# Optimization experiments

Measured on AMD Instinct MI355X. Metric: run time of the kernel, lower is better.

The kernel has to match this reference:

```python
import jax, jax.numpy as jnp
import numpy as np

E, D, H, R = 8, 2048, 8192, 64   # experts, d_model(in=out), hidden, rank
N = 4096                          # tokens (batch*seq)


def setup_inputs() -> dict:
    key = jax.random.key(0)
    ks = jax.random.split(key, 8)
    f32 = jnp.float32
    x = jax.random.normal(ks[0], (N, D), f32)
    # Stacked low-rank expert params: expert i = relu(x@u1@v1+b1) @ u2 @ v2 + b2
    u1 = jax.random.normal(ks[1], (E, D, R), f32) / np.float32(np.sqrt(D))
    v1 = jax.random.normal(ks[2], (E, R, H), f32) / np.float32(np.sqrt(R))
    b1 = jnp.zeros((E, H), f32)
    u2 = jax.random.normal(ks[3], (E, H, R), f32) / np.float32(np.sqrt(H))
    v2 = jax.random.normal(ks[4], (E, R, D), f32) / np.float32(np.sqrt(R))
    b2 = jnp.zeros((E, D), f32)
    # gate = nn.Linear(D, E): weight [E, D], bias [E]
    gate_w = jax.random.normal(ks[5], (E, D), f32) / np.float32(np.sqrt(D))
    gate_b = jnp.zeros((E,), f32)
    return dict(x=x, u1=u1, v1=v1, b1=b1, u2=u2, v2=v2, b2=b2,
                gate_w=gate_w, gate_b=gate_b)


def reference(x, u1, v1, b1, u2, v2, b2, gate_w, gate_b):
    # --- routing: softmax gate, top-2, renormalize ---
    logits = x @ gate_w.T + gate_b                      # [N, E]
    probs = jax.nn.softmax(logits, axis=-1)
    top_p, top_i = jax.lax.top_k(probs, 2)              # [N, 2]
    top_p = top_p / jnp.sum(top_p, axis=-1, keepdims=True)
    # combine weight per (token, expert): zero unless expert in top-2
    w = jnp.sum(jax.nn.one_hot(top_i, E, dtype=x.dtype) * top_p[..., None], axis=1)  # [N, E]

    # --- experts: low-rank MLP applied per expert, weighted accumulate ---
    def body(acc, params):
        u1e, v1e, b1e, u2e, v2e, b2e, we = params       # we: [N]
        h = jax.nn.relu((x @ u1e) @ v1e + b1e)          # [N, H]
        y = (h @ u2e) @ v2e + b2e                       # [N, D]
        return acc + we[:, None] * y, None

    out, _ = jax.lax.scan(body, jnp.zeros_like(x), (u1, v1, b1, u2, v2, b2, w.T))
    return out
```

## Files before the change

kernel.cpp:

```cpp
#include <hip/hip_runtime.h>
#include <hip/hip_bf16.h>

#define E 8
#define D 2048
#define H 8192
#define R 64
#define NTOK 4096
#define HSPLIT 4
#define HPER (H / HSPLIT)

typedef __attribute__((ext_vector_type(8))) short bf16x8;
typedef __attribute__((ext_vector_type(4))) float f32x4;

__device__ __forceinline__ unsigned short f2b(float f){
  union { __hip_bfloat16 h; unsigned short u; } cv;
  cv.h = __float2bfloat16(f);
  return cv.u;
}
__device__ __forceinline__ float b2f(unsigned short u){
  union { unsigned int i; float f; } cv; cv.i = ((unsigned int)u) << 16; return cv.f;
}

__device__ __forceinline__ bf16x8 ldfrag(const unsigned short* base, int row0, int k0,
                                         int pitch, int lane){
  return *reinterpret_cast<const bf16x8*>(base + (row0 + (lane & 15)) * pitch
                                          + k0 + ((lane >> 4) << 3));
}

__global__ __launch_bounds__(256) void pack_tr(const float* __restrict__ src,
                                               unsigned short* __restrict__ dst,
                                               int RS, int CS){
  int e = blockIdx.z;
  const float* s = src + (size_t)e * RS * CS;
  unsigned short* d = dst + (size_t)e * RS * CS;
  int c0 = blockIdx.x * 64, r0 = blockIdx.y * 64;
  int l = threadIdx.x & 63, cb = (threadIdx.x >> 6) * 16;
  int r = r0 + l;
  const float4* sp = reinterpret_cast<const float4*>(s + (size_t)r * CS + c0 + cb);
  float v[16];
  #pragma unroll
  for (int q = 0; q < 4; ++q){
    float4 t = sp[q];
    v[q*4] = t.x; v[q*4+1] = t.y; v[q*4+2] = t.z; v[q*4+3] = t.w;
  }
  #pragma unroll
  for (int j = 0; j < 16; ++j)
    d[(size_t)(c0 + cb + j) * RS + r] = f2b(v[j]);
}

__global__ __launch_bounds__(256) void gate_kernel(
    const float* __restrict__ x, const float* __restrict__ gw,
    const float* __restrict__ gb, int* __restrict__ cnt,
    int* __restrict__ lst, int* __restrict__ tsl,
    unsigned short* __restrict__ xb)
{
  int wid  = threadIdx.x >> 6;
  int lane = threadIdx.x & 63;
  int n0 = blockIdx.x * 16 + wid * 4;

  float acc[4][E];
  #pragma unroll
  for (int t = 0; t < 4; ++t)
    #pragma unroll
    for (int e = 0; e < E; ++e) acc[t][e] = 0.f;

  for (int i = 0; i < D / 256; ++i){
    int dd = i * 256 + lane * 4;
    float4 xv[4];
    #pragma unroll
    for (int t = 0; t < 4; ++t){
      xv[t] = *reinterpret_cast<const float4*>(x + (size_t)(n0 + t) * D + dd);
      unsigned short o[4] = { f2b(xv[t].x), f2b(xv[t].y), f2b(xv[t].z), f2b(xv[t].w) };
      *reinterpret_cast<ushort4*>(xb + (size_t)(n0 + t) * D + dd) = *reinterpret_cast<ushort4*>(o);
    }
    #pragma unroll
    for (int e = 0; e < E; ++e){
      float4 g = *reinterpret_cast<const float4*>(gw + (size_t)e * D + dd);
      #pragma unroll
      for (int t = 0; t < 4; ++t)
        acc[t][e] += xv[t].x * g.x + xv[t].y * g.y + xv[t].z * g.z + xv[t].w * g.w;
    }
  }

  #pragma unroll
  for (int t = 0; t < 4; ++t){
    #pragma unroll
    for (int e = 0; e < E; ++e){
      float v = acc[t][e];
      for (int off = 32; off; off >>= 1) v += __shfl_xor(v, off, 64);
      acc[t][e] = v + gb[e];
    }
    if (lane == 0){
      int n = n0 + t;
      float l0 = -1e30f, l1 = -1e30f; int i0 = 0, i1 = 0;
      #pragma unroll
      for (int e = 0; e < E; ++e){
        float v = acc[t][e];
        if (v > l0){ l1 = l0; i1 = i0; l0 = v; i0 = e; }
        else if (v > l1){ l1 = v; i1 = e; }
      }
      float tt = expf(l1 - l0);
      float w0 = 1.f / (1.f + tt);
      float w1 = tt * w0;
      int p0 = atomicAdd(&cnt[i0], 1);
      lst[i0 * NTOK + p0] = n;
      int p1 = atomicAdd(&cnt[i1], 1);
      lst[i1 * NTOK + p1] = n;
      int* ts = tsl + n * 8;
      ts[0] = i0; ts[1] = p0; ts[2] = __float_as_int(w0);
      ts[3] = i1; ts[4] = p1; ts[5] = __float_as_int(w1);
    }
  }
}

__global__ __launch_bounds__(256) void t1_kernel(
    const unsigned short* __restrict__ xb, const unsigned short* __restrict__ u1p,
    const int* __restrict__ cnt, const int* __restrict__ lst,
    unsigned short* __restrict__ T1buf)
{
  int e = blockIdx.y;
  int nc = cnt[e];
  int t0 = blockIdx.x * 64;
  if (t0 >= nc) return;

  __shared__ int s_tok[64];
  __shared__ unsigned short Xs[64 * 136];
  __shared__ unsigned short U1s[64 * 136];
  int tid = threadIdx.x, w = tid >> 6, lane = tid & 63;

  if (tid < 64) s_tok[tid] = lst[e * NTOK + min(t0 + tid, nc - 1)];
  __syncthreads();

  int m = (w & 3) * 16;
  f32x4 z = {0.f, 0.f, 0.f, 0.f};
  f32x4 acc[4] = {z, z, z, z};

  for (int kc = 0; kc < D; kc += 128){
    __syncthreads();
    #pragma unroll
    for (int s = 0; s < 4; ++s){
      int id = tid + s * 256;
      int rr = id >> 4, c = (id & 15) * 8;
      *reinterpret_cast<bf16x8*>(&Xs[rr * 136 + c]) =
        *reinterpret_cast<const bf16x8*>(&xb[(size_t)s_tok[rr] * D + kc + c]);
      *reinterpret_cast<bf16x8*>(&U1s[rr * 136 + c]) =
        *reinterpret_cast<const bf16x8*>(&u1p[((size_t)e * R + rr) * D + kc + c]);
    }
    __syncthreads();
    #pragma unroll
    for (int j = 0; j < 4; ++j)
      #pragma unroll
      for (int ks = 0; ks < 4; ++ks)
        acc[j] = __builtin_amdgcn_mfma_f32_16x16x32_bf16(
            ldfrag(Xs, m, ks * 32, 136, lane),
            ldfrag(U1s, j * 16, ks * 32, 136, lane), acc[j], 0, 0, 0);
  }
  #pragma unroll
  for (int j = 0; j < 4; ++j){
    int col = j * 16 + (lane & 15);
    #pragma unroll
    for (int q = 0; q < 4; ++q){
      int row = m + ((lane >> 4) << 2) + q;
      T1buf[((size_t)e * NTOK + t0 + row) * R + col] = f2b(acc[j][q]);
    }
  }
}

__global__ __launch_bounds__(512, 4) void mid_kernel(
    const unsigned short* __restrict__ T1buf, const unsigned short* __restrict__ v1p,
    const unsigned short* __restrict__ u2p, const float* __restrict__ b1,
    const int* __restrict__ cnt, float* __restrict__ T2acc)
{
  int e = blockIdx.z;
  int nc = cnt[e];
  int t0 = blockIdx.x * 64;
  if (t0 >= nc) return;
  int hc0 = blockIdx.y * HPER;

  __shared__ unsigned short T1s[64 * 72];
  __shared__ unsigned short v1s[128 * 72];
  __shared__ unsigned short u2s[64 * 136];
  __shared__ unsigned short Hs[64 * 136];
  __shared__ float b1s[HPER];

  int tid = threadIdx.x, w = tid >> 6, lane = tid & 63;

  { int rr = tid >> 3, c = (tid & 7) * 8;
    *reinterpret_cast<bf16x8*>(&T1s[rr * 72 + c]) =
      *reinterpret_cast<const bf16x8*>(&T1buf[((size_t)e * NTOK + t0 + rr) * R + c]); }
  for (int i = tid; i < HPER; i += 512) b1s[i] = b1[(size_t)e * H + hc0 + i];

  int m1 = (w & 1) * 32, n1 = (w >> 1) * 32;
  int m2 = (w & 3) * 16, r2 = (w >> 2) * 32;
  f32x4 z = {0.f, 0.f, 0.f, 0.f};
  f32x4 acc[2] = {z, z};

  bf16x8 pv[2], pu[2];
  #pragma unroll
  for (int s = 0; s < 2; ++s){
    int id = tid + s * 512;
    pv[s] = *reinterpret_cast<const bf16x8*>(&v1p[((size_t)e * H + hc0 + (id >> 3)) * R + (id & 7) * 8]);
    pu[s] = *reinterpret_cast<const bf16x8*>(&u2p[((size_t)e * R + (id >> 4)) * H + hc0 + (id & 15) * 8]);
  }

  for (int hs = 0; hs < HPER; hs += 128){
    __syncthreads();
    #pragma unroll
    for (int s = 0; s < 2; ++s){
      int id = tid + s * 512;
      *reinterpret_cast<bf16x8*>(&v1s[(id >> 3) * 72 + (id & 7) * 8]) = pv[s];
      *reinterpret_cast<bf16x8*>(&u2s[(id >> 4) * 136 + (id & 15) * 8]) = pu[s];
    }
    __syncthreads();
    #pragma unroll
    for (int i = 0; i < 2; ++i)
      #pragma unroll
      for (int j = 0; j < 2; ++j){
        f32x4 a = z;
        #pragma unroll
        for (int ks = 0; ks < 2; ++ks)
          a = __builtin_amdgcn_mfma_f32_16x16x32_bf16(
              ldfrag(T1s, m1 + i * 16, ks * 32, 72, lane),
              ldfrag(v1s, n1 + j * 16, ks * 32, 72, lane), a, 0, 0, 0);
        int hcol = n1 + j * 16 + (lane & 15);
        float bv = b1s[hs + hcol];
        #pragma unroll
        for (int q = 0; q < 4; ++q){
          float vv = a[q] + bv;
          Hs[(m1 + i * 16 + ((lane >> 4) << 2) + q) * 136 + hcol] = f2b(vv > 0.f ? vv : 0.f);
        }
      }
    int hn = (hs + 128 < HPER) ? hs + 128 : 0;
    #pragma unroll
    for (int s = 0; s < 2; ++s){
      int id = tid + s * 512;
      pv[s] = *reinterpret_cast<const bf16x8*>(&v1p[((size_t)e * H + hc0 + hn + (id >> 3)) * R + (id & 7) * 8]);
      pu[s] = *reinterpret_cast<const bf16x8*>(&u2p[((size_t)e * R + (id >> 4)) * H + hc0 + hn + (id & 15) * 8]);
    }
    __syncthreads();
    #pragma unroll
    for (int j = 0; j < 2; ++j)
      #pragma unroll
      for (int ks = 0; ks < 4; ++ks)
        acc[j] = __builtin_amdgcn_mfma_f32_16x16x32_bf16(
            ldfrag(Hs, m2, ks * 32, 136, lane),
            ldfrag(u2s, r2 + j * 16, ks * 32, 136, lane), acc[j], 0, 0, 0);
  }
  #pragma unroll
  for (int j = 0; j < 2; ++j){
    int col = r2 + j * 16 + (lane & 15);
    #pragma unroll
    for (int q = 0; q < 4; ++q){
      int row = m2 + ((lane >> 4) << 2) + q;
      atomicAdd(&T2acc[((size_t)e * NTOK + t0 + row) * R + col], acc[j][q]);
    }
  }
}

__global__ __launch_bounds__(512, 4) void out_kernel(
    const float* __restrict__ T2acc, const unsigned short* __restrict__ v2p,
    const float* __restrict__ b2, const int* __restrict__ cnt,
    unsigned short* __restrict__ yb)
{
  int e = blockIdx.y;
  int nc = cnt[e];
  int t0 = blockIdx.x * 64;
  if (t0 >= nc) return;
  int base = 0;
  #pragma unroll
  for (int i = 0; i < E; ++i) base += (i < e) ? cnt[i] : 0;

  __shared__ unsigned short T2s[64 * 72];
  __shared__ unsigned short v2s[256 * 72];
  __shared__ float b2s[D];
  int tid = threadIdx.x, w = tid >> 6, lane = tid & 63;

  { int rr = tid >> 3, c = (tid & 7) * 8;
    const float* src = &T2acc[((size_t)e * NTOK + t0 + rr) * R + c];
    float4 a = *reinterpret_cast<const float4*>(src);
    float4 b = *reinterpret_cast<const float4*>(src + 4);
    unsigned short o[8] = { f2b(a.x), f2b(a.y), f2b(a.z), f2b(a.w),
                            f2b(b.x), f2b(b.y), f2b(b.z), f2b(b.w) };
    *reinterpret_cast<bf16x8*>(&T2s[rr * 72 + c]) = *reinterpret_cast<bf16x8*>(o); }
  for (int i = tid; i < D; i += 512) b2s[i] = b2[(size_t)e * D + i];

  int m1 = (w & 1) * 32, nb = (w >> 1) * 64;
  f32x4 z = {0.f, 0.f, 0.f, 0.f};

  for (int dc = 0; dc < D; dc += 256){
    __syncthreads();
    #pragma unroll
    for (int s = 0; s < 4; ++s){
      int id = tid + s * 512;
      int rr = id >> 3, c = (id & 7) * 8;
      *reinterpret_cast<bf16x8*>(&v2s[rr * 72 + c]) =
        *reinterpret_cast<const bf16x8*>(&v2p[((size_t)e * D + dc + rr) * R + c]);
    }
    __syncthreads();
    #pragma unroll
    for (int i = 0; i < 2; ++i)
      #pragma unroll
      for (int j = 0; j < 4; ++j){
        f32x4 a = z;
        #pragma unroll
        for (int ks = 0; ks < 2; ++ks)
          a = __builtin_amdgcn_mfma_f32_16x16x32_bf16(
              ldfrag(T2s, m1 + i * 16, ks * 32, 72, lane),
              ldfrag(v2s, nb + j * 16, ks * 32, 72, lane), a, 0, 0, 0);
        int dcol = dc + nb + j * 16 + (lane & 15);
        float bv = b2s[dcol];
        #pragma unroll
        for (int q = 0; q < 4; ++q){
          int row = m1 + i * 16 + ((lane >> 4) << 2) + q;
          if (t0 + row < nc)
            yb[((size_t)(base + t0 + row)) * D + dcol] = f2b(a[q] + bv);
        }
      }
  }
}

__global__ __launch_bounds__(256) void combine_kernel(
    const unsigned short* __restrict__ yb, const int* __restrict__ tsl,
    const int* __restrict__ cnt, float* __restrict__ out)
{
  int tok = blockIdx.x;
  int d0 = threadIdx.x * 8;
  const int* ts = tsl + tok * 8;
  int e0 = ts[0], p0 = ts[1]; float w0 = __int_as_float(ts[2]);
  int e1 = ts[3], p1 = ts[4]; float w1 = __int_as_float(ts[5]);
  int b0 = 0, b1s = 0;
  #pragma unroll
  for (int i = 0; i < E; ++i){
    int c = cnt[i];
    b0  += (i < e0) ? c : 0;
    b1s += (i < e1) ? c : 0;
  }
  bf16x8 y0 = *reinterpret_cast<const bf16x8*>(&yb[((size_t)(b0 + p0)) * D + d0]);
  bf16x8 y1 = *reinterpret_cast<const bf16x8*>(&yb[((size_t)(b1s + p1)) * D + d0]);
  float o[8];
  #pragma unroll
  for (int j = 0; j < 8; ++j)
    o[j] = w0 * b2f((unsigned short)y0[j]) + w1 * b2f((unsigned short)y1[j]);
  *reinterpret_cast<float4*>(&out[(size_t)tok * D + d0])     = *reinterpret_cast<float4*>(&o[0]);
  *reinterpret_cast<float4*>(&out[(size_t)tok * D + d0 + 4]) = *reinterpret_cast<float4*>(&o[4]);
}

extern "C" void kernel_launch(void* const* d_in, const int* in_sizes, int n_in,
                              void* d_out, int out_size, void* d_ws, size_t ws_size,
                              hipStream_t stream)
{
  const float* x  = (const float*)d_in[0];
  const float* u1 = (const float*)d_in[1];
  const float* v1 = (const float*)d_in[2];
  const float* b1 = (const float*)d_in[3];
  const float* u2 = (const float*)d_in[4];
  const float* v2 = (const float*)d_in[5];
  const float* b2 = (const float*)d_in[6];
  const float* gw = (const float*)d_in[7];
  const float* gb = (const float*)d_in[8];
  float* out = (float*)d_out;

  const size_t SZ_XB  = (size_t)NTOK * D * 2;
  const size_t SZ_U1P = (size_t)E * R * D * 2;
  const size_t SZ_V1P = (size_t)E * H * R * 2;
  const size_t SZ_U2P = (size_t)E * R * H * 2;
  const size_t SZ_V2P = (size_t)E * D * R * 2;
  const size_t SZ_T1  = (size_t)E * NTOK * R * 2;
  const size_t SZ_T2  = (size_t)E * NTOK * R * 4;

  char* ws = (char*)d_ws;
  size_t o = 0;
  auto take = [&](size_t b){ void* p = ws + o; o = (o + b + 255) & ~(size_t)255; return p; };
  int* cnt = (int*)take(E * 4);
  int* lst = (int*)take((size_t)E * NTOK * 4);
  int* tsl = (int*)take((size_t)NTOK * 8 * 4);
  char* A  = (char*)take(SZ_XB + SZ_U1P + SZ_V1P + SZ_U2P);
  unsigned short* xb  = (unsigned short*)A;
  unsigned short* u1p = (unsigned short*)(A + SZ_XB);
  unsigned short* v1p = (unsigned short*)(A + SZ_XB + SZ_U1P);
  unsigned short* u2p = (unsigned short*)(A + SZ_XB + SZ_U1P + SZ_V1P);
  unsigned short* yb  = (unsigned short*)A;
  unsigned short* v2p = (unsigned short*)take(SZ_V2P);
  unsigned short* T1buf = (unsigned short*)take(SZ_T1);
  float* T2acc = (float*)take(SZ_T2);

  hipMemsetAsync(cnt, 0, E * 4, stream);
  hipMemsetAsync(T2acc, 0, SZ_T2, stream);

  gate_kernel<<<NTOK / 16, 256, 0, stream>>>(x, gw, gb, cnt, lst, tsl, xb);
  pack_tr<<<dim3(1, D / 64, E), 256, 0, stream>>>(u1, u1p, D, R);
  pack_tr<<<dim3(H / 64, 1, E), 256, 0, stream>>>(v1, v1p, R, H);
  pack_tr<<<dim3(1, H / 64, E), 256, 0, stream>>>(u2, u2p, H, R);
  pack_tr<<<dim3(D / 64, 1, E), 256, 0, stream>>>(v2, v2p, R, D);

  t1_kernel<<<dim3(NTOK / 64, E), 256, 0, stream>>>(xb, u1p, cnt, lst, T1buf);
  mid_kernel<<<dim3(NTOK / 64, HSPLIT, E), 512, 0, stream>>>(T1buf, v1p, u2p, b1, cnt, T2acc);
  out_kernel<<<dim3(NTOK / 64, E), 512, 0, stream>>>(T2acc, v2p, b2, cnt, yb);
  combine_kernel<<<NTOK, 256, 0, stream>>>(yb, tsl, cnt, out);
}
```

Baseline: 367.0 us.

## Split routing into wave-aggregated route kernel and halve gate tokens per block

Moves the per-expert slot assignment out of the gate kernel into a separate route kernel. There, each wave uses ballots and popcounts to reserve slots with one atomic per expert per wave, replacing two global atomics per token. The gate kernel now handles 2 tokens per wave instead of 4, doubling the grid for more parallelism. The cost is an extra kernel launch and a round trip of routing data through global memory.

```diff
diff --git a/kernel.cpp b/kernel.cpp
--- a/kernel.cpp
+++ b/kernel.cpp
@@ -50,25 +50,24 @@
 
 __global__ __launch_bounds__(256) void gate_kernel(
     const float* __restrict__ x, const float* __restrict__ gw,
-    const float* __restrict__ gb, int* __restrict__ cnt,
-    int* __restrict__ lst, int* __restrict__ tsl,
+    const float* __restrict__ gb, int* __restrict__ tsl,
     unsigned short* __restrict__ xb)
 {
   int wid  = threadIdx.x >> 6;
   int lane = threadIdx.x & 63;
-  int n0 = blockIdx.x * 16 + wid * 4;
-
-  float acc[4][E];
-  #pragma unroll
-  for (int t = 0; t < 4; ++t)
+  int n0 = blockIdx.x * 8 + wid * 2;
+
+  float acc[2][E];
+  #pragma unroll
+  for (int t = 0; t < 2; ++t)
     #pragma unroll
     for (int e = 0; e < E; ++e) acc[t][e] = 0.f;
 
   for (int i = 0; i < D / 256; ++i){
     int dd = i * 256 + lane * 4;
-    float4 xv[4];
-    #pragma unroll
-    for (int t = 0; t < 4; ++t){
+    float4 xv[2];
+    #pragma unroll
+    for (int t = 0; t < 2; ++t){
       xv[t] = *reinterpret_cast<const float4*>(x + (size_t)(n0 + t) * D + dd);
       unsigned short o[4] = { f2b(xv[t].x), f2b(xv[t].y), f2b(xv[t].z), f2b(xv[t].w) };
       *reinterpret_cast<ushort4*>(xb + (size_t)(n0 + t) * D + dd) = *reinterpret_cast<ushort4*>(o);
@@ -77,13 +76,13 @@
     for (int e = 0; e < E; ++e){
       float4 g = *reinterpret_cast<const float4*>(gw + (size_t)e * D + dd);
       #pragma unroll
-      for (int t = 0; t < 4; ++t)
+      for (int t = 0; t < 2; ++t)
         acc[t][e] += xv[t].x * g.x + xv[t].y * g.y + xv[t].z * g.z + xv[t].w * g.w;
     }
   }
 
   #pragma unroll
-  for (int t = 0; t < 4; ++t){
+  for (int t = 0; t < 2; ++t){
     #pragma unroll
     for (int e = 0; e < E; ++e){
       float v = acc[t][e];
@@ -102,13 +101,39 @@
       float tt = expf(l1 - l0);
       float w0 = 1.f / (1.f + tt);
       float w1 = tt * w0;
-      int p0 = atomicAdd(&cnt[i0], 1);
-      lst[i0 * NTOK + p0] = n;
-      int p1 = atomicAdd(&cnt[i1], 1);
-      lst[i1 * NTOK + p1] = n;
       int* ts = tsl + n * 8;
-      ts[0] = i0; ts[1] = p0; ts[2] = __float_as_int(w0);
-      ts[3] = i1; ts[4] = p1; ts[5] = __float_as_int(w1);
+      ts[0] = i0; ts[2] = __float_as_int(w0);
+      ts[3] = i1; ts[5] = __float_as_int(w1);
+    }
+  }
+}
+
+__global__ __launch_bounds__(256) void route_kernel(
+    int* __restrict__ tsl, int* __restrict__ cnt, int* __restrict__ lst)
+{
+  int wid  = threadIdx.x >> 6;
+  int lane = threadIdx.x & 63;
+  int tok  = blockIdx.x * 256 + wid * 64 + lane;
+  int* ts = tsl + tok * 8;
+  int i0 = ts[0], i1 = ts[3];
+  unsigned long long below = (1ULL << lane) - 1ULL;
+
+  #pragma unroll
+  for (int e = 0; e < E; ++e){
+    unsigned long long m0 = __ballot(i0 == e);
+    unsigned long long m1 = __ballot(i1 == e);
+    int c0  = __popcll(m0);
+    int tot = c0 + __popcll(m1);
+    int base = 0;
+    if (lane == 0 && tot) base = atomicAdd(&cnt[e], tot);
+    base = __shfl(base, 0, 64);
+    if (i0 == e){
+      int p = base + __popcll(m0 & below);
+      lst[e * NTOK + p] = tok;  ts[1] = p;
+    }
+    if (i1 == e){
+      int p = base + c0 + __popcll(m1 & below);
+      lst[e * NTOK + p] = tok;  ts[4] = p;
     }
   }
 }
@@ -387,7 +412,8 @@
   hipMemsetAsync(cnt, 0, E * 4, stream);
   hipMemsetAsync(T2acc, 0, SZ_T2, stream);
 
-  gate_kernel<<<NTOK / 16, 256, 0, stream>>>(x, gw, gb, cnt, lst, tsl, xb);
+  gate_kernel<<<NTOK / 8, 256, 0, stream>>>(x, gw, gb, tsl, xb);
+  route_kernel<<<NTOK / 256, 256, 0, stream>>>(tsl, cnt, lst);
   pack_tr<<<dim3(1, D / 64, E), 256, 0, stream>>>(u1, u1p, D, R);
   pack_tr<<<dim3(H / 64, 1, E), 256, 0, stream>>>(v1, v1p, R, H);
   pack_tr<<<dim3(1, H / 64, E), 256, 0, stream>>>(u2, u2p, H, R);
```

Result: faster. 309.8 us (-15.6%).
